# Performance work log

Measured on AMD Instinct MI355X. Metric: run time of the kernel, lower is better.

Reference implementation:

```python
import jax, jax.numpy as jnp
import numpy as np


def sine_encode_2d(pos, d):
    # pos: (..., 2) normalized relative positions in [-1, 1]; output (..., d)
    # standard sinusoidal encoding per coordinate, d/2 dims each (sin/cos pairs)
    d_half = d // 2
    n_freq = d_half // 2
    freqs = jnp.exp(-jnp.log(jnp.float32(10000.0)) * jnp.arange(n_freq, dtype=jnp.float32) / n_freq)
    parts = []
    for i in range(2):
        ang = pos[..., i:i + 1] * freqs  # (..., n_freq)
        parts.append(jnp.sin(ang))
        parts.append(jnp.cos(ang))
    return jnp.concatenate(parts, axis=-1)


def rpe_bias(W_rpe, t_q, f_q, t_k, f_k, N_t, N_f, d_rpe):
    dt_norm = jnp.arange(-(N_t - 1), N_t, dtype=jnp.float32) / max(N_t - 1, 1)
    df_norm = jnp.arange(-(N_f - 1), N_f, dtype=jnp.float32) / max(N_f - 1, 1)
    DT, DF = jnp.meshgrid(dt_norm, df_norm, indexing='ij')       # (2Nt-1, 2Nf-1)
    rel = jnp.stack([DT, DF], axis=-1)                            # (2Nt-1, 2Nf-1, 2)
    enc = sine_encode_2d(rel, d_rpe)                              # (2Nt-1, 2Nf-1, d_rpe)
    table = enc @ W_rpe.T                                         # (2Nt-1, 2Nf-1, h)
    n_df = 2 * N_f - 1
    flat = table.reshape(-1, table.shape[-1])                     # ((2Nt-1)*(2Nf-1), h)
    dt_idx = t_q[:, None] - t_k[None, :] + (N_t - 1)              # (Nq, Nk)
    df_idx = f_q[:, None] - f_k[None, :] + (N_f - 1)
    flat_idx = jnp.clip(dt_idx * n_df + df_idx, 0, flat.shape[0] - 1)
    bias = flat[flat_idx]                                         # (Nq, Nk, h)
    return jnp.transpose(bias, (2, 0, 1))                         # (h, Nq, Nk)


def setup_inputs() -> dict:
    key = jax.random.key(0)
    ks = jax.random.split(key, 12)
    B, N_t, N_f, d_model, n_heads, d_rpe = 8, 14, 72, 256, 8, 32
    N = N_t * N_f
    s = 1.0 / np.sqrt(d_model)
    return {
        'q_tokens': jax.random.normal(ks[0], (B, N, d_model), jnp.float32),
        'k_tokens': jax.random.normal(ks[1], (B, N, d_model), jnp.float32),
        'v_tokens': jax.random.normal(ks[2], (B, N, d_model), jnp.float32),
        't_q': jax.random.randint(ks[3], (N,), 0, N_t),
        'f_q': jax.random.randint(ks[4], (N,), 0, N_f),
        't_k': jax.random.randint(ks[5], (N,), 0, N_t),
        'f_k': jax.random.randint(ks[6], (N,), 0, N_f),
        'N_t': N_t,
        'N_f': N_f,
        'W_q': jax.random.normal(ks[7], (d_model, d_model), jnp.float32) * s,
        'W_k': jax.random.normal(ks[8], (d_model, d_model), jnp.float32) * s,
        'W_v': jax.random.normal(ks[9], (d_model, d_model), jnp.float32) * s,
        'W_o': jax.random.normal(ks[10], (d_model, d_model), jnp.float32) * s,
        'W_rpe': jax.random.normal(ks[11], (n_heads, d_rpe), jnp.float32) * (1.0 / np.sqrt(d_rpe)),
    }


def reference(q_tokens, k_tokens, v_tokens, t_q, f_q, t_k, f_k, N_t, N_f,
              W_q, W_k, W_v, W_o, W_rpe):
    B, N_q, d_model = q_tokens.shape
    N_k = k_tokens.shape[1]
    h = W_rpe.shape[0]
    d_rpe = W_rpe.shape[1]
    dk = d_model // h
    scale = jnp.float32(np.sqrt(dk))
    Q = (q_tokens @ W_q.T).reshape(B, N_q, h, dk)
    K = (k_tokens @ W_k.T).reshape(B, N_k, h, dk)
    V = (v_tokens @ W_v.T).reshape(B, N_k, h, dk)
    scores = jnp.einsum('bqhd,bkhd->bhqk', Q, K) / scale          # (B, h, Nq, Nk)
    bias = rpe_bias(W_rpe, t_q, f_q, t_k, f_k, N_t, N_f, d_rpe)   # (h, Nq, Nk)
    attn = jax.nn.softmax(scores + bias[None], axis=-1)
    out = jnp.einsum('bhqk,bkhd->bqhd', attn, V).reshape(B, N_q, d_model)
    return out @ W_o.T
```

## Files before the change

kernel.cpp:

```cpp
#include <hip/hip_runtime.h>

#define B_    8
#define N_    1008
#define D_    256
#define H_    8
#define DK_   32
#define DA_   64
#define BND_  (B_*N_*D_)
#define L2E_  1.4426950408889634f

typedef _Float16 half8_t __attribute__((ext_vector_type(8)));
typedef _Float16 half4_t __attribute__((ext_vector_type(4)));
typedef float    f32x4   __attribute__((ext_vector_type(4)));

#if defined(__has_builtin)
#if __has_builtin(__builtin_amdgcn_exp2f)
#define EXP2(x) __builtin_amdgcn_exp2f(x)
#else
#define EXP2(x) exp2f(x)
#endif
#else
#define EXP2(x) exp2f(x)
#endif

__global__ void prep_kernel(const int* __restrict__ t_q, const int* __restrict__ f_q,
                            const int* __restrict__ t_k, const int* __restrict__ f_k,
                            const float* __restrict__ W_rpe,
                            _Float16* __restrict__ Qa, _Float16* __restrict__ Ka)
{
    const float FR[8] = {1.f, 0.31622776601683794f, 0.1f, 0.03162277660168379f,
                         0.01f, 0.0031622776601683794f, 0.001f, 0.00031622776601683794f};
    int id = blockIdx.x * 256 + threadIdx.x;
    if (id < N_ * H_) {
        int q = id >> 3, h = id & 7;
        float tq = (float)t_q[q] * (1.f / 13.f);
        float fq = (float)f_q[q] * (1.f / 71.f);
        const float* Wh = W_rpe + h * 32;
        half8_t u0, u1, u2, u3;
#pragma unroll
        for (int i = 0; i < 8; i++) {
            float sa = sinf(tq * FR[i]), ca = cosf(tq * FR[i]);
            float sb = sinf(fq * FR[i]), cb = cosf(fq * FR[i]);
            u0[i] = (_Float16)(L2E_ * (Wh[i] * sa + Wh[8 + i] * ca));
            u1[i] = (_Float16)(L2E_ * (Wh[8 + i] * sa - Wh[i] * ca));
            u2[i] = (_Float16)(L2E_ * (Wh[16 + i] * sb + Wh[24 + i] * cb));
            u3[i] = (_Float16)(L2E_ * (Wh[24 + i] * sb - Wh[16 + i] * cb));
        }
#pragma unroll
        for (int b = 0; b < 8; b++) {
            _Float16* dst = &Qa[(((size_t)(b * 8 + h)) * N_ + q) * DA_ + 32];
            *(half8_t*)(dst + 0) = u0;  *(half8_t*)(dst + 8) = u1;
            *(half8_t*)(dst + 16) = u2; *(half8_t*)(dst + 24) = u3;
        }
    } else if (id < N_ * H_ + N_ * 64) {
        int id2 = id - N_ * H_;
        int k = id2 >> 6, bh = id2 & 63;
        float tk = (float)t_k[k] * (1.f / 13.f);
        float fk = (float)f_k[k] * (1.f / 71.f);
        half8_t v0, v1, v2, v3;
#pragma unroll
        for (int i = 0; i < 8; i++) {
            v0[i] = (_Float16)cosf(tk * FR[i]);
            v1[i] = (_Float16)sinf(tk * FR[i]);
            v2[i] = (_Float16)cosf(fk * FR[i]);
            v3[i] = (_Float16)sinf(fk * FR[i]);
        }
        _Float16* dst = &Ka[(((size_t)bh) * N_ + k) * DA_ + 32];
        *(half8_t*)(dst + 0) = v0;  *(half8_t*)(dst + 8) = v1;
        *(half8_t*)(dst + 16) = v2; *(half8_t*)(dst + 24) = v3;
    }
}

__global__ __launch_bounds__(256, 2) void qkv_gemm(
    const float* __restrict__ q_tok, const float* __restrict__ k_tok,
    const float* __restrict__ v_tok, const float* __restrict__ Wq,
    const float* __restrict__ Wk, const float* __restrict__ Wv,
    _Float16* __restrict__ Qa, _Float16* __restrict__ Ka, _Float16* __restrict__ Vt)
{
    __shared__ __align__(16) _Float16 fw[8 * 8 * 64 * 8];
    const int tid = threadIdx.x;
    const int lane = tid & 63, w = tid >> 6, quad = lane >> 4, l15 = lane & 15;
    const int z = blockIdx.z;
    const int m0 = blockIdx.x * 128, n0 = blockIdx.y * 128;
    const float* A = (z == 0) ? q_tok : (z == 1) ? k_tok : v_tok;
    const float* W = (z == 0) ? Wq : (z == 1) ? Wk : Wv;

#pragma unroll
    for (int p = 0; p < 16; p++) {
        int g = p * 256 + tid;
        int ch = g >> 9, rem = g & 511, nt = rem >> 6, L = rem & 63;
        const float* src = &W[(size_t)(n0 + nt * 16 + (L & 15)) * D_ + ch * 32 + ((L >> 4) & 3) * 8];
        float4 w0 = *(const float4*)src;
        float4 w1 = *(const float4*)(src + 4);
        half8_t hv = {(_Float16)w0.x, (_Float16)w0.y, (_Float16)w0.z, (_Float16)w0.w,
                      (_Float16)w1.x, (_Float16)w1.y, (_Float16)w1.z, (_Float16)w1.w};
        *(half8_t*)&fw[g * 8] = hv;
    }
    __syncthreads();

    f32x4 acc[2][8] = {};
    const float* Ar0 = &A[(size_t)(m0 + w * 16 + l15) * D_];
    const float* Ar1 = Ar0 + (size_t)64 * D_;
#pragma unroll
    for (int ch = 0; ch < 8; ch++) {
        float4 a00 = *(const float4*)&Ar0[ch * 32 + quad * 8];
        float4 a01 = *(const float4*)&Ar0[ch * 32 + quad * 8 + 4];
        float4 a10 = *(const float4*)&Ar1[ch * 32 + quad * 8];
        float4 a11 = *(const float4*)&Ar1[ch * 32 + quad * 8 + 4];
        half8_t af0 = {(_Float16)a00.x, (_Float16)a00.y, (_Float16)a00.z, (_Float16)a00.w,
                       (_Float16)a01.x, (_Float16)a01.y, (_Float16)a01.z, (_Float16)a01.w};
        half8_t af1 = {(_Float16)a10.x, (_Float16)a10.y, (_Float16)a10.z, (_Float16)a10.w,
                       (_Float16)a11.x, (_Float16)a11.y, (_Float16)a11.z, (_Float16)a11.w};
#pragma unroll
        for (int nt = 0; nt < 8; nt++) {
            half8_t bf = *(const half8_t*)&fw[((ch * 8 + nt) * 64 + lane) * 8];
            acc[0][nt] = __builtin_amdgcn_mfma_f32_16x16x32_f16(af0, bf, acc[0][nt], 0, 0, 0);
            acc[1][nt] = __builtin_amdgcn_mfma_f32_16x16x32_f16(af1, bf, acc[1][nt], 0, 0, 0);
        }
    }
    const float scale = (z == 0) ? 0.17677669529663687f * L2E_ : 1.0f;
#pragma unroll
    for (int mt = 0; mt < 2; mt++) {
        int mbase = m0 + mt * 64 + w * 16 + quad * 4;
        int b = mbase / N_;
        int q = mbase - b * N_;
        if (z < 2) {
            _Float16* out = (z == 0) ? Qa : Ka;
#pragma unroll
            for (int nt = 0; nt < 8; nt++) {
                int n = n0 + nt * 16 + l15;
                int hh = n >> 5, d = n & 31;
                _Float16* dst = &out[(((size_t)(b * 8 + hh)) * N_ + q) * DA_ + d];
#pragma unroll
                for (int r = 0; r < 4; r++)
                    dst[(size_t)r * DA_] = (_Float16)(acc[mt][nt][r] * scale);
            }
        } else {
#pragma unroll
            for (int nt = 0; nt < 8; nt++) {
                int n = n0 + nt * 16 + l15;
                int hh = n >> 5, d = n & 31;
                half4_t o = {(_Float16)acc[mt][nt][0], (_Float16)acc[mt][nt][1],
                             (_Float16)acc[mt][nt][2], (_Float16)acc[mt][nt][3]};
                *(half4_t*)&Vt[(((size_t)(b * 8 + hh)) * DK_ + d) * N_ + q] = o;
            }
        }
    }
}

__global__ __launch_bounds__(256, 4) void attn(const _Float16* __restrict__ Qa,
    const _Float16* __restrict__ Ka, const _Float16* __restrict__ Vt,
    _Float16* __restrict__ AO)
{
    __shared__ __align__(16) _Float16 fk[2][4096];
    __shared__ __align__(16) _Float16 fv[2][2048];
    __shared__ __align__(16) _Float16 plds[4][16][72];

    const int tid = threadIdx.x;
    const int lane = tid & 63, w = tid >> 6, quad = lane >> 4, l15 = lane & 15;
    const int bh = blockIdx.y, q0 = blockIdx.x * 64;
    const int b = bh >> 3, hh = bh & 7;
    const _Float16* Kb = Ka + (size_t)bh * N_ * DA_;
    const _Float16* Vb = Vt + (size_t)bh * DK_ * N_;

    const int s_l15 = tid & 15, s_quad = (tid >> 4) & 3;
    const int s_mt = tid >> 6;
    const int s_c = tid >> 7;
    const int s_mt2 = (tid >> 6) & 1;

    const int qg = q0 + w * 16 + l15;
    const int qc = qg < N_ ? qg : N_ - 1;
    const _Float16* Qrow = &Qa[((size_t)bh * N_ + qc) * DA_];
    half8_t qf0 = *(const half8_t*)&Qrow[quad * 8];
    half8_t qf1 = *(const half8_t*)&Qrow[32 + quad * 8];

    float m_run = -1e30f, l_run = 0.f;
    f32x4 O[2] = {};

    {
        int krow = s_mt * 16 + s_l15;
        *(half8_t*)&fk[0][((s_mt * 2 + 0) * 64 + lane) * 8] =
            *(const half8_t*)&Kb[(size_t)krow * DA_ + s_quad * 8];
        *(half8_t*)&fk[0][((s_mt * 2 + 1) * 64 + lane) * 8] =
            *(const half8_t*)&Kb[(size_t)krow * DA_ + 32 + s_quad * 8];
        int vrow = s_mt2 * 16 + s_l15;
        int vcol = s_c * 32 + s_quad * 8;
        *(half8_t*)&fv[0][tid * 8] = *(const half8_t*)&Vb[(size_t)vrow * N_ + vcol];
    }
    __syncthreads();

    for (int kt = 0; kt < 16; kt++) {
        const int cb = kt & 1;
        if (kt < 15) {
            int k0n = (kt + 1) * 64;
            int krow = k0n + s_mt * 16 + s_l15;
            if (krow > N_ - 1) krow = N_ - 1;
            *(half8_t*)&fk[cb ^ 1][((s_mt * 2 + 0) * 64 + lane) * 8] =
                *(const half8_t*)&Kb[(size_t)krow * DA_ + s_quad * 8];
            *(half8_t*)&fk[cb ^ 1][((s_mt * 2 + 1) * 64 + lane) * 8] =
                *(const half8_t*)&Kb[(size_t)krow * DA_ + 32 + s_quad * 8];
            int vrow = s_mt2 * 16 + s_l15;
            int vcol = k0n + s_c * 32 + s_quad * 8;
            if (vcol > N_ - 8) vcol = N_ - 8;
            *(half8_t*)&fv[cb ^ 1][tid * 8] = *(const half8_t*)&Vb[(size_t)vrow * N_ + vcol];
        }
        f32x4 S[4];
#pragma unroll
        for (int mt = 0; mt < 4; mt++) {
            half8_t kf0 = *(const half8_t*)&fk[cb][((mt * 2 + 0) * 64 + lane) * 8];
            half8_t kf1 = *(const half8_t*)&fk[cb][((mt * 2 + 1) * 64 + lane) * 8];
            f32x4 zz = {0.f, 0.f, 0.f, 0.f};
            zz = __builtin_amdgcn_mfma_f32_16x16x32_f16(kf0, qf0, zz, 0, 0, 0);
            S[mt] = __builtin_amdgcn_mfma_f32_16x16x32_f16(kf1, qf1, zz, 0, 0, 0);
        }
        if (kt == 15)
            S[3] = (f32x4){-1e30f, -1e30f, -1e30f, -1e30f};
        float tmax = -1e30f;
#pragma unroll
        for (int mt = 0; mt < 4; mt++)
#pragma unroll
            for (int r = 0; r < 4; r++) tmax = fmaxf(tmax, S[mt][r]);
        tmax = fmaxf(tmax, __shfl_xor(tmax, 16, 64));
        tmax = fmaxf(tmax, __shfl_xor(tmax, 32, 64));
        float mnew = fmaxf(m_run, tmax);
        float alpha = EXP2(m_run - mnew);
        m_run = mnew;
        float tsum = 0.f;
#pragma unroll
        for (int mt = 0; mt < 4; mt++) {
            float p0 = EXP2(S[mt][0] - mnew), p1 = EXP2(S[mt][1] - mnew);
            float p2 = EXP2(S[mt][2] - mnew), p3 = EXP2(S[mt][3] - mnew);
            tsum += (p0 + p1) + (p2 + p3);
            half4_t ph = {(_Float16)p0, (_Float16)p1, (_Float16)p2, (_Float16)p3};
            *(half4_t*)&plds[w][l15][mt * 16 + quad * 4] = ph;
        }
        tsum += __shfl_xor(tsum, 16, 64);
        tsum += __shfl_xor(tsum, 32, 64);
        l_run = l_run * alpha + tsum;
        O[0] = O[0] * alpha;
        O[1] = O[1] * alpha;
#pragma unroll
        for (int c = 0; c < 2; c++) {
            half8_t pf = *(const half8_t*)&plds[w][l15][c * 32 + quad * 8];
            half8_t vfa = *(const half8_t*)&fv[cb][((c * 2 + 0) * 64 + lane) * 8];
            half8_t vfb = *(const half8_t*)&fv[cb][((c * 2 + 1) * 64 + lane) * 8];
            O[0] = __builtin_amdgcn_mfma_f32_16x16x32_f16(vfa, pf, O[0], 0, 0, 0);
            O[1] = __builtin_amdgcn_mfma_f32_16x16x32_f16(vfb, pf, O[1], 0, 0, 0);
        }
        __syncthreads();
    }
    if (qg < N_) {
        float inv = 1.f / l_run;
#pragma unroll
        for (int mt2 = 0; mt2 < 2; mt2++) {
            half4_t o = {(_Float16)(O[mt2][0] * inv), (_Float16)(O[mt2][1] * inv),
                         (_Float16)(O[mt2][2] * inv), (_Float16)(O[mt2][3] * inv)};
            *(half4_t*)&AO[((size_t)b * N_ + qg) * D_ + hh * DK_ + mt2 * 16 + quad * 4] = o;
        }
    }
}

__global__ __launch_bounds__(256, 2) void out_gemm(const _Float16* __restrict__ A,
    const float* __restrict__ W, float* __restrict__ out)
{
    __shared__ __align__(16) _Float16 fw[8 * 8 * 64 * 8];
    const int tid = threadIdx.x;
    const int lane = tid & 63, w = tid >> 6, quad = lane >> 4, l15 = lane & 15;
    const int m0 = blockIdx.x * 128, n0 = blockIdx.y * 128;

#pragma unroll
    for (int p = 0; p < 16; p++) {
        int g = p * 256 + tid;
        int ch = g >> 9, rem = g & 511, nt = rem >> 6, L = rem & 63;
        const float* src = &W[(size_t)(n0 + nt * 16 + (L & 15)) * D_ + ch * 32 + ((L >> 4) & 3) * 8];
        float4 w0 = *(const float4*)src;
        float4 w1 = *(const float4*)(src + 4);
        half8_t hv = {(_Float16)w0.x, (_Float16)w0.y, (_Float16)w0.z, (_Float16)w0.w,
                      (_Float16)w1.x, (_Float16)w1.y, (_Float16)w1.z, (_Float16)w1.w};
        *(half8_t*)&fw[g * 8] = hv;
    }
    __syncthreads();

    f32x4 acc[2][8] = {};
    const _Float16* Ar0 = &A[(size_t)(m0 + w * 16 + l15) * D_];
    const _Float16* Ar1 = Ar0 + (size_t)64 * D_;
#pragma unroll
    for (int ch = 0; ch < 8; ch++) {
        half8_t af0 = *(const half8_t*)&Ar0[ch * 32 + quad * 8];
        half8_t af1 = *(const half8_t*)&Ar1[ch * 32 + quad * 8];
#pragma unroll
        for (int nt = 0; nt < 8; nt++) {
            half8_t bf = *(const half8_t*)&fw[((ch * 8 + nt) * 64 + lane) * 8];
            acc[0][nt] = __builtin_amdgcn_mfma_f32_16x16x32_f16(af0, bf, acc[0][nt], 0, 0, 0);
            acc[1][nt] = __builtin_amdgcn_mfma_f32_16x16x32_f16(af1, bf, acc[1][nt], 0, 0, 0);
        }
    }
#pragma unroll
    for (int mt = 0; mt < 2; mt++) {
        int mbase = m0 + mt * 64 + w * 16 + quad * 4;
#pragma unroll
        for (int nt = 0; nt < 8; nt++) {
            int n = n0 + nt * 16 + l15;
#pragma unroll
            for (int r = 0; r < 4; r++)
                out[(size_t)(mbase + r) * D_ + n] = acc[mt][nt][r];
        }
    }
}

extern "C" void kernel_launch(void* const* d_in, const int* in_sizes, int n_in,
                              void* d_out, int out_size, void* d_ws, size_t ws_size,
                              hipStream_t stream)
{
    const float* q_tokens = (const float*)d_in[0];
    const float* k_tokens = (const float*)d_in[1];
    const float* v_tokens = (const float*)d_in[2];
    const int*   t_q      = (const int*)d_in[3];
    const int*   f_q      = (const int*)d_in[4];
    const int*   t_k      = (const int*)d_in[5];
    const int*   f_k      = (const int*)d_in[6];
    const float* W_q   = (const float*)d_in[9];
    const float* W_k   = (const float*)d_in[10];
    const float* W_v   = (const float*)d_in[11];
    const float* W_o   = (const float*)d_in[12];
    const float* W_rpe = (const float*)d_in[13];

    _Float16* ws = (_Float16*)d_ws;
    _Float16* Qa = ws;
    _Float16* Ka = Qa + (size_t)64 * N_ * DA_;
    _Float16* Vt = Ka + (size_t)64 * N_ * DA_;
    _Float16* AO = Vt + (size_t)64 * DK_ * N_;

    prep_kernel<<<dim3(284), 256, 0, stream>>>(t_q, f_q, t_k, f_k, W_rpe, Qa, Ka);
    qkv_gemm<<<dim3(63, 2, 3), 256, 0, stream>>>(q_tokens, k_tokens, v_tokens,
                                                 W_q, W_k, W_v, Qa, Ka, Vt);
    attn<<<dim3(16, 64), 256, 0, stream>>>(Qa, Ka, Vt, AO);
    out_gemm<<<dim3(63, 2), 256, 0, stream>>>(AO, W_o, (float*)d_out);
}
```

Measured before the change: 167.8 us.

## Prefetch global loads into registers, reorder attention grid, use fast trig in prep

```diff
diff --git a/kernel.cpp b/kernel.cpp
--- a/kernel.cpp
+++ b/kernel.cpp
@@ -39,8 +39,8 @@
         half8_t u0, u1, u2, u3;
 #pragma unroll
         for (int i = 0; i < 8; i++) {
-            float sa = sinf(tq * FR[i]), ca = cosf(tq * FR[i]);
-            float sb = sinf(fq * FR[i]), cb = cosf(fq * FR[i]);
+            float sa = __sinf(tq * FR[i]), ca = __cosf(tq * FR[i]);
+            float sb = __sinf(fq * FR[i]), cb = __cosf(fq * FR[i]);
             u0[i] = (_Float16)(L2E_ * (Wh[i] * sa + Wh[8 + i] * ca));
             u1[i] = (_Float16)(L2E_ * (Wh[8 + i] * sa - Wh[i] * ca));
             u2[i] = (_Float16)(L2E_ * (Wh[16 + i] * sb + Wh[24 + i] * cb));
@@ -52,22 +52,26 @@
             *(half8_t*)(dst + 0) = u0;  *(half8_t*)(dst + 8) = u1;
             *(half8_t*)(dst + 16) = u2; *(half8_t*)(dst + 24) = u3;
         }
-    } else if (id < N_ * H_ + N_ * 64) {
+    } else {
         int id2 = id - N_ * H_;
-        int k = id2 >> 6, bh = id2 & 63;
+        int k = id2 >> 3, o = id2 & 7;
         float tk = (float)t_k[k] * (1.f / 13.f);
         float fk = (float)f_k[k] * (1.f / 71.f);
         half8_t v0, v1, v2, v3;
 #pragma unroll
         for (int i = 0; i < 8; i++) {
-            v0[i] = (_Float16)cosf(tk * FR[i]);
-            v1[i] = (_Float16)sinf(tk * FR[i]);
-            v2[i] = (_Float16)cosf(fk * FR[i]);
-            v3[i] = (_Float16)sinf(fk * FR[i]);
-        }
-        _Float16* dst = &Ka[(((size_t)bh) * N_ + k) * DA_ + 32];
-        *(half8_t*)(dst + 0) = v0;  *(half8_t*)(dst + 8) = v1;
-        *(half8_t*)(dst + 16) = v2; *(half8_t*)(dst + 24) = v3;
+            v0[i] = (_Float16)__cosf(tk * FR[i]);
+            v1[i] = (_Float16)__sinf(tk * FR[i]);
+            v2[i] = (_Float16)__cosf(fk * FR[i]);
+            v3[i] = (_Float16)__sinf(fk * FR[i]);
+        }
+#pragma unroll
+        for (int j = 0; j < 8; j++) {
+            int bh = o * 8 + j;
+            _Float16* dst = &Ka[(((size_t)bh) * N_ + k) * DA_ + 32];
+            *(half8_t*)(dst + 0) = v0;  *(half8_t*)(dst + 8) = v1;
+            *(half8_t*)(dst + 16) = v2; *(half8_t*)(dst + 24) = v3;
+        }
     }
 }
 
@@ -84,6 +88,13 @@
     const int m0 = blockIdx.x * 128, n0 = blockIdx.y * 128;
     const float* A = (z == 0) ? q_tok : (z == 1) ? k_tok : v_tok;
     const float* W = (z == 0) ? Wq : (z == 1) ? Wk : Wv;
+
+    const float* Ar0 = &A[(size_t)(m0 + w * 16 + l15) * D_];
+    const float* Ar1 = Ar0 + (size_t)64 * D_;
+    float4 a00 = *(const float4*)&Ar0[quad * 8];
+    float4 a01 = *(const float4*)&Ar0[quad * 8 + 4];
+    float4 a10 = *(const float4*)&Ar1[quad * 8];
+    float4 a11 = *(const float4*)&Ar1[quad * 8 + 4];
 
 #pragma unroll
     for (int p = 0; p < 16; p++) {
@@ -99,18 +110,18 @@
     __syncthreads();
 
     f32x4 acc[2][8] = {};
-    const float* Ar0 = &A[(size_t)(m0 + w * 16 + l15) * D_];
-    const float* Ar1 = Ar0 + (size_t)64 * D_;
 #pragma unroll
     for (int ch = 0; ch < 8; ch++) {
-        float4 a00 = *(const float4*)&Ar0[ch * 32 + quad * 8];
-        float4 a01 = *(const float4*)&Ar0[ch * 32 + quad * 8 + 4];
-        float4 a10 = *(const float4*)&Ar1[ch * 32 + quad * 8];
-        float4 a11 = *(const float4*)&Ar1[ch * 32 + quad * 8 + 4];
         half8_t af0 = {(_Float16)a00.x, (_Float16)a00.y, (_Float16)a00.z, (_Float16)a00.w,
                        (_Float16)a01.x, (_Float16)a01.y, (_Float16)a01.z, (_Float16)a01.w};
         half8_t af1 = {(_Float16)a10.x, (_Float16)a10.y, (_Float16)a10.z, (_Float16)a10.w,
                        (_Float16)a11.x, (_Float16)a11.y, (_Float16)a11.z, (_Float16)a11.w};
+        if (ch < 7) {
+            a00 = *(const float4*)&Ar0[(ch + 1) * 32 + quad * 8];
+            a01 = *(const float4*)&Ar0[(ch + 1) * 32 + quad * 8 + 4];
+            a10 = *(const float4*)&Ar1[(ch + 1) * 32 + quad * 8];
+            a11 = *(const float4*)&Ar1[(ch + 1) * 32 + quad * 8 + 4];
+        }
 #pragma unroll
         for (int nt = 0; nt < 8; nt++) {
             half8_t bf = *(const half8_t*)&fw[((ch * 8 + nt) * 64 + lane) * 8];
@@ -158,7 +169,7 @@
 
     const int tid = threadIdx.x;
     const int lane = tid & 63, w = tid >> 6, quad = lane >> 4, l15 = lane & 15;
-    const int bh = blockIdx.y, q0 = blockIdx.x * 64;
+    const int bh = blockIdx.x, q0 = blockIdx.y * 64;
     const int b = bh >> 3, hh = bh & 7;
     const _Float16* Kb = Ka + (size_t)bh * N_ * DA_;
     const _Float16* Vb = Vt + (size_t)bh * DK_ * N_;
@@ -191,20 +202,20 @@
 
     for (int kt = 0; kt < 16; kt++) {
         const int cb = kt & 1;
+        half8_t nk0, nk1, nv;
         if (kt < 15) {
             int k0n = (kt + 1) * 64;
             int krow = k0n + s_mt * 16 + s_l15;
             if (krow > N_ - 1) krow = N_ - 1;
-            *(half8_t*)&fk[cb ^ 1][((s_mt * 2 + 0) * 64 + lane) * 8] =
-                *(const half8_t*)&Kb[(size_t)krow * DA_ + s_quad * 8];
-            *(half8_t*)&fk[cb ^ 1][((s_mt * 2 + 1) * 64 + lane) * 8] =
-                *(const half8_t*)&Kb[(size_t)krow * DA_ + 32 + s_quad * 8];
+            nk0 = *(const half8_t*)&Kb[(size_t)krow * DA_ + s_quad * 8];
+            nk1 = *(const half8_t*)&Kb[(size_t)krow * DA_ + 32 + s_quad * 8];
             int vrow = s_mt2 * 16 + s_l15;
             int vcol = k0n + s_c * 32 + s_quad * 8;
             if (vcol > N_ - 8) vcol = N_ - 8;
-            *(half8_t*)&fv[cb ^ 1][tid * 8] = *(const half8_t*)&Vb[(size_t)vrow * N_ + vcol];
+            nv = *(const half8_t*)&Vb[(size_t)vrow * N_ + vcol];
         }
         f32x4 S[4];
+        __builtin_amdgcn_s_setprio(1);
 #pragma unroll
         for (int mt = 0; mt < 4; mt++) {
             half8_t kf0 = *(const half8_t*)&fk[cb][((mt * 2 + 0) * 64 + lane) * 8];
@@ -213,13 +224,14 @@
             zz = __builtin_amdgcn_mfma_f32_16x16x32_f16(kf0, qf0, zz, 0, 0, 0);
             S[mt] = __builtin_amdgcn_mfma_f32_16x16x32_f16(kf1, qf1, zz, 0, 0, 0);
         }
+        __builtin_amdgcn_s_setprio(0);
         if (kt == 15)
             S[3] = (f32x4){-1e30f, -1e30f, -1e30f, -1e30f};
-        float tmax = -1e30f;
-#pragma unroll
-        for (int mt = 0; mt < 4; mt++)
-#pragma unroll
-            for (int r = 0; r < 4; r++) tmax = fmaxf(tmax, S[mt][r]);
+        float x0 = fmaxf(fmaxf(S[0][0], S[0][1]), fmaxf(S[0][2], S[0][3]));
+        float x1 = fmaxf(fmaxf(S[1][0], S[1][1]), fmaxf(S[1][2], S[1][3]));
+        float x2 = fmaxf(fmaxf(S[2][0], S[2][1]), fmaxf(S[2][2], S[2][3]));
+        float x3 = fmaxf(fmaxf(S[3][0], S[3][1]), fmaxf(S[3][2], S[3][3]));
+        float tmax = fmaxf(fmaxf(x0, x1), fmaxf(x2, x3));
         tmax = fmaxf(tmax, __shfl_xor(tmax, 16, 64));
         tmax = fmaxf(tmax, __shfl_xor(tmax, 32, 64));
         float mnew = fmaxf(m_run, tmax);
@@ -239,6 +251,7 @@
         l_run = l_run * alpha + tsum;
         O[0] = O[0] * alpha;
         O[1] = O[1] * alpha;
+        __builtin_amdgcn_s_setprio(1);
 #pragma unroll
         for (int c = 0; c < 2; c++) {
             half8_t pf = *(const half8_t*)&plds[w][l15][c * 32 + quad * 8];
@@ -247,6 +260,12 @@
             O[0] = __builtin_amdgcn_mfma_f32_16x16x32_f16(vfa, pf, O[0], 0, 0, 0);
             O[1] = __builtin_amdgcn_mfma_f32_16x16x32_f16(vfb, pf, O[1], 0, 0, 0);
         }
+        __builtin_amdgcn_s_setprio(0);
+        if (kt < 15) {
+            *(half8_t*)&fk[cb ^ 1][((s_mt * 2 + 0) * 64 + lane) * 8] = nk0;
+            *(half8_t*)&fk[cb ^ 1][((s_mt * 2 + 1) * 64 + lane) * 8] = nk1;
+            *(half8_t*)&fv[cb ^ 1][tid * 8] = nv;
+        }
         __syncthreads();
     }
     if (qg < N_) {
@@ -267,6 +286,11 @@
     const int tid = threadIdx.x;
     const int lane = tid & 63, w = tid >> 6, quad = lane >> 4, l15 = lane & 15;
     const int m0 = blockIdx.x * 128, n0 = blockIdx.y * 128;
+
+    const _Float16* Ar0 = &A[(size_t)(m0 + w * 16 + l15) * D_];
+    const _Float16* Ar1 = Ar0 + (size_t)64 * D_;
+    half8_t af0 = *(const half8_t*)&Ar0[quad * 8];
+    half8_t af1 = *(const half8_t*)&Ar1[quad * 8];
 
 #pragma unroll
     for (int p = 0; p < 16; p++) {
@@ -282,17 +306,18 @@
     __syncthreads();
 
     f32x4 acc[2][8] = {};
-    const _Float16* Ar0 = &A[(size_t)(m0 + w * 16 + l15) * D_];
-    const _Float16* Ar1 = Ar0 + (size_t)64 * D_;
 #pragma unroll
     for (int ch = 0; ch < 8; ch++) {
-        half8_t af0 = *(const half8_t*)&Ar0[ch * 32 + quad * 8];
-        half8_t af1 = *(const half8_t*)&Ar1[ch * 32 + quad * 8];
+        half8_t c0 = af0, c1 = af1;
+        if (ch < 7) {
+            af0 = *(const half8_t*)&Ar0[(ch + 1) * 32 + quad * 8];
+            af1 = *(const half8_t*)&Ar1[(ch + 1) * 32 + quad * 8];
+        }
 #pragma unroll
         for (int nt = 0; nt < 8; nt++) {
             half8_t bf = *(const half8_t*)&fw[((ch * 8 + nt) * 64 + lane) * 8];
-            acc[0][nt] = __builtin_amdgcn_mfma_f32_16x16x32_f16(af0, bf, acc[0][nt], 0, 0, 0);
-            acc[1][nt] = __builtin_amdgcn_mfma_f32_16x16x32_f16(af1, bf, acc[1][nt], 0, 0, 0);
+            acc[0][nt] = __builtin_amdgcn_mfma_f32_16x16x32_f16(c0, bf, acc[0][nt], 0, 0, 0);
+            acc[1][nt] = __builtin_amdgcn_mfma_f32_16x16x32_f16(c1, bf, acc[1][nt], 0, 0, 0);
         }
     }
 #pragma unroll
@@ -331,9 +356,9 @@
     _Float16* Vt = Ka + (size_t)64 * N_ * DA_;
     _Float16* AO = Vt + (size_t)64 * DK_ * N_;
 
-    prep_kernel<<<dim3(284), 256, 0, stream>>>(t_q, f_q, t_k, f_k, W_rpe, Qa, Ka);
+    prep_kernel<<<dim3(63), 256, 0, stream>>>(t_q, f_q, t_k, f_k, W_rpe, Qa, Ka);
     qkv_gemm<<<dim3(63, 2, 3), 256, 0, stream>>>(q_tokens, k_tokens, v_tokens,
                                                  W_q, W_k, W_v, Qa, Ka, Vt);
-    attn<<<dim3(16, 64), 256, 0, stream>>>(Qa, Ka, Vt, AO);
+    attn<<<dim3(64, 16), 256, 0, stream>>>(Qa, Ka, Vt, AO);
     out_gemm<<<dim3(63, 2), 256, 0, stream>>>(AO, W_o, (float*)d_out);
 }
```

Measured after the change: 154.3 us. -8.1%, faster.
